# Kernel optimization log

Hardware: AMD Instinct MI355X
Metric: run time of the kernel (lower is better)

Reference implementation:

```python
import jax, jax.numpy as jnp
import numpy as np

GROUP_SIZE = 64

def _dequant_w4(qweight, wscales):
    """Unpack int4 weights and apply per-(group, out-channel) scales.
    qweight: [N, K//2] uint8-valued ints, low nibble = even k, high nibble = odd k.
    wscales: [K//GROUP_SIZE, N] float. Returns [N, K] float weight.
    """
    q = qweight.astype(jnp.int32)
    low = (q & 15) - 8          # [N, K//2], signed int4
    high = ((q >> 4) & 15) - 8  # [N, K//2]
    N = q.shape[0]
    K = q.shape[1] * 2
    w_int = jnp.stack([low, high], axis=-1).reshape(N, K)  # interleaved low/high
    # scale[n, k] = wscales[k // GROUP_SIZE, n]
    scale = jnp.repeat(wscales, GROUP_SIZE, axis=0).T  # [N, K]
    return w_int.astype(wscales.dtype) * scale

def setup_inputs() -> dict:
    key = jax.random.key(0)
    ks = jax.random.split(key, 7)
    M, K, N, R = 8192, 4096, 4096, 32
    x = jax.random.normal(ks[0], (M, K), dtype=jnp.float32)
    qweight = jax.random.randint(ks[1], (N, K // 2), 0, 256, dtype=jnp.int32)
    wscales = jax.random.uniform(ks[2], (K // GROUP_SIZE, N), dtype=jnp.float32) * 0.01 + 0.001
    proj_down = jax.random.normal(ks[3], (R, K), dtype=jnp.float32) * 0.02
    proj_up = jax.random.normal(ks[4], (N, R), dtype=jnp.float32) * 0.02
    wtscale = jnp.ones((1,), dtype=jnp.float32)
    bias = jax.random.normal(ks[5], (N,), dtype=jnp.float32) * 0.01
    return {"x": x, "qweight": qweight, "wscales": wscales,
            "proj_down": proj_down, "proj_up": proj_up,
            "wtscale": wtscale, "bias": bias}

def reference(x, qweight, wscales, proj_down, proj_up, wtscale, bias):
    # Dequant int4 weight, GEMM, low-rank LoRA correction scaled by wtscale, bias.
    w = _dequant_w4(qweight, wscales)              # [N, K]
    out = x @ w.T                                  # [M, N]
    lora = (x @ proj_down.T) @ proj_up.T           # [M, R] @ [R, N] -> [M, N]
    out = out + lora * wtscale
    out = out + bias
    return out
```

## Files before the change

kernel.cpp:

```cpp
#include <hip/hip_runtime.h>
#include <hip/hip_bf16.h>
#include <stdint.h>

#define MD 8192
#define ND 4096
#define KD 4096
#define RD 32

typedef __bf16 bf16x8 __attribute__((ext_vector_type(8)));
typedef float f32x4 __attribute__((ext_vector_type(4)));

__device__ __forceinline__ void cp16(const void* g, void* l) {
    __builtin_amdgcn_global_load_lds(
        (const __attribute__((address_space(1))) void*)g,
        (__attribute__((address_space(3))) void*)l, 16, 0, 0);
}

__global__ __launch_bounds__(256) void cvt_x(const float* __restrict__ x,
                                             __hip_bfloat16* __restrict__ y) {
    size_t i = ((size_t)blockIdx.x * 256 + threadIdx.x) * 8;
    float4 a = *(const float4*)(x + i);
    float4 b = *(const float4*)(x + i + 4);
    union { __hip_bfloat16 h[8]; uint4 u; } o;
    o.h[0] = __float2bfloat16(a.x); o.h[1] = __float2bfloat16(a.y);
    o.h[2] = __float2bfloat16(a.z); o.h[3] = __float2bfloat16(a.w);
    o.h[4] = __float2bfloat16(b.x); o.h[5] = __float2bfloat16(b.y);
    o.h[6] = __float2bfloat16(b.z); o.h[7] = __float2bfloat16(b.w);
    *(uint4*)(y + i) = o.u;
}

__global__ __launch_bounds__(256) void build_weff(
    const int* __restrict__ qw,
    const float* __restrict__ wsc,
    const float* __restrict__ pd,
    const float* __restrict__ pu,
    const float* __restrict__ wts_p,
    __hip_bfloat16* __restrict__ weff)
{
    __shared__ float pd_s[RD][132];
    __shared__ float pu_t[RD][68];
    const int t = threadIdx.x;
    const int kb = blockIdx.x * 128;
    const int nb = blockIdx.y * 64;

    for (int f = t; f < (RD * 128) / 4; f += 256) {
        int r = f >> 5;
        int c = (f & 31) << 2;
        *(float4*)&pd_s[r][c] = *(const float4*)(pd + (size_t)r * KD + kb + c);
    }
    for (int f = t; f < (64 * RD) / 4; f += 256) {
        int nl = f >> 3;
        int r4 = (f & 7) << 2;
        float4 v = *(const float4*)(pu + (size_t)(nb + nl) * RD + r4);
        pu_t[r4 + 0][nl] = v.x; pu_t[r4 + 1][nl] = v.y;
        pu_t[r4 + 2][nl] = v.z; pu_t[r4 + 3][nl] = v.w;
    }
    __syncthreads();

    const float wts = wts_p[0];
    const int kc = (t & 15) << 3;
    const int ng = (t >> 4) << 2;

    float acc[4][8];
#pragma unroll
    for (int i = 0; i < 4; ++i)
#pragma unroll
        for (int j = 0; j < 8; ++j) acc[i][j] = 0.f;

    for (int r = 0; r < RD; ++r) {
        float4 pda = *(const float4*)&pd_s[r][kc];
        float4 pdb = *(const float4*)&pd_s[r][kc + 4];
        float4 puv = *(const float4*)&pu_t[r][ng];
        float pus[4] = {puv.x, puv.y, puv.z, puv.w};
        float pdv[8] = {pda.x, pda.y, pda.z, pda.w, pdb.x, pdb.y, pdb.z, pdb.w};
#pragma unroll
        for (int i = 0; i < 4; ++i)
#pragma unroll
            for (int j = 0; j < 8; ++j)
                acc[i][j] += pus[i] * pdv[j];
    }

    const int kg = kb + kc;
    const int g = kg >> 6;
#pragma unroll
    for (int i = 0; i < 4; ++i) {
        const int n = nb + ng + i;
        const float sc = wsc[(size_t)g * ND + n];
        int4 q = *(const int4*)(qw + (size_t)n * (KD / 2) + (kg >> 1));
        const int qi[4] = {q.x, q.y, q.z, q.w};
        union { __hip_bfloat16 h[8]; uint4 u; } o;
#pragma unroll
        for (int j = 0; j < 4; ++j) {
            const int lo = (qi[j] & 15) - 8;
            const int hi = ((qi[j] >> 4) & 15) - 8;
            o.h[2 * j]     = __float2bfloat16((float)lo * sc + wts * acc[i][2 * j]);
            o.h[2 * j + 1] = __float2bfloat16((float)hi * sc + wts * acc[i][2 * j + 1]);
        }
        *(uint4*)(weff + (size_t)n * KD + kg) = o.u;
    }
}

#define FENCE asm volatile("" ::: "memory")

#define PHASEH(CB, SL)                                                         \
    {                                                                          \
        bf16x8 af[8], bf[4];                                                   \
        _Pragma("unroll") for (int i = 0; i < 8; ++i)                          \
            af[i] = *(const bf16x8*)(ArowB + (CB) + i * 2048 + (SL));          \
        _Pragma("unroll") for (int j = 0; j < 4; ++j)                          \
            bf[j] = *(const bf16x8*)(BrowB + (CB) + j * 2048 + (SL));          \
        asm volatile("s_waitcnt lgkmcnt(0)" ::: "memory");                     \
        __builtin_amdgcn_sched_barrier(0);                                     \
        __builtin_amdgcn_s_setprio(1);                                         \
        _Pragma("unroll") for (int i = 0; i < 8; ++i)                          \
            _Pragma("unroll") for (int j = 0; j < 4; ++j)                      \
                acc[i][j] = __builtin_amdgcn_mfma_f32_16x16x32_bf16(           \
                    af[i], bf[j], acc[i][j], 0, 0, 0);                         \
        __builtin_amdgcn_s_setprio(0);                                         \
    }

__global__ __launch_bounds__(512, 2) void gemm_bt_bias(
    const __hip_bfloat16* __restrict__ A,
    const __hip_bfloat16* __restrict__ B,
    const float* __restrict__ bias,
    float* __restrict__ C)
{
    __shared__ alignas(16) char As[2][32768];
    __shared__ alignas(16) char Bs[2][32768];

    const int t = threadIdx.x;
    const int lane = t & 63;
    const int w = t >> 6;
    const int wm = w >> 2;
    const int wn = w & 3;

    const int bid = blockIdx.x;
    const int swz = (bid & 7) * 64 + (bid >> 3);
    const int m0 = (swz >> 4) * 256;
    const int n0 = (swz & 15) * 256;

    const int lrow = lane >> 3;
    const int gch = (lane & 7) ^ lrow;
    const __hip_bfloat16* Ag = A + (size_t)(m0 + lrow) * KD + gch * 8;
    const __hip_bfloat16* Bg = B + (size_t)(n0 + lrow) * KD + gch * 8;

    const int qm = lane & 15;
    const int c4 = lane >> 4;
    const int slh0 = (c4 ^ (qm & 7)) * 16;
    const int slh1 = ((4 + c4) ^ (qm & 7)) * 16;
    const char* ArowB = (const char*)As + (wm * 128 + qm) * 128;
    const char* BrowB = (const char*)Bs + (wn * 64 + qm) * 128;

    f32x4 acc[8][4];
#pragma unroll
    for (int i = 0; i < 8; ++i)
#pragma unroll
        for (int j = 0; j < 4; ++j) acc[i][j] = (f32x4){0.f, 0.f, 0.f, 0.f};

#pragma unroll
    for (int q = 0; q < 4; ++q) {
        const int blk = w + 8 * q;
        cp16(Ag + (size_t)blk * 8 * KD, (char*)As + blk * 1024);
        cp16(Bg + (size_t)blk * 8 * KD, (char*)Bs + blk * 1024);
    }
    asm volatile("s_waitcnt vmcnt(0)" ::: "memory");
    __builtin_amdgcn_s_barrier();
    FENCE;

    for (int kt = 0; kt < 63; ++kt) {
        const int cb = (kt & 1) << 15;
        const int sb = cb ^ 32768;
        const size_t ko = (size_t)(kt + 1) * 64;
#pragma unroll
        for (int q = 0; q < 4; ++q) {
            const int blk = w + 8 * q;
            cp16(Ag + (size_t)blk * 8 * KD + ko, (char*)As + sb + blk * 1024);
            cp16(Bg + (size_t)blk * 8 * KD + ko, (char*)Bs + sb + blk * 1024);
        }
        PHASEH(cb, slh0)
        PHASEH(cb, slh1)
        asm volatile("s_waitcnt vmcnt(0)" ::: "memory");
        __builtin_amdgcn_s_barrier();
        FENCE;
    }
    PHASEH(32768, slh0)
    PHASEH(32768, slh1)

    const int cm = (lane >> 4) << 2;
    const int cn = lane & 15;
#pragma unroll
    for (int j = 0; j < 4; ++j) {
        const int n = n0 + wn * 64 + j * 16 + cn;
        const float bv = bias[n];
#pragma unroll
        for (int i = 0; i < 8; ++i) {
            float* dst = C + (size_t)(m0 + wm * 128 + i * 16 + cm) * ND + n;
#pragma unroll
            for (int r = 0; r < 4; ++r)
                dst[(size_t)r * ND] = acc[i][j][r] + bv;
        }
    }
}

extern "C" void kernel_launch(void* const* d_in, const int* in_sizes, int n_in,
                              void* d_out, int out_size, void* d_ws, size_t ws_size,
                              hipStream_t stream) {
    const float* x    = (const float*)d_in[0];
    const int* qw     = (const int*)d_in[1];
    const float* wsc  = (const float*)d_in[2];
    const float* pd   = (const float*)d_in[3];
    const float* pu   = (const float*)d_in[4];
    const float* wts  = (const float*)d_in[5];
    const float* bias = (const float*)d_in[6];
    float* out = (float*)d_out;

    __hip_bfloat16* weff = (__hip_bfloat16*)d_ws;
    __hip_bfloat16* xbf  = (__hip_bfloat16*)((char*)d_ws + (size_t)ND * KD * sizeof(__hip_bfloat16));

    cvt_x<<<(MD * (size_t)KD) / (256 * 8), 256, 0, stream>>>(x, xbf);
    build_weff<<<dim3(KD / 128, ND / 64), 256, 0, stream>>>(qw, wsc, pd, pu, wts, weff);
    gemm_bt_bias<<<512, 512, 0, stream>>>(xbf, weff, bias, out);
}
```

Before: 553.7 us.

## Split GEMM k-loop into quadrant phases interleaving loads, barriers and MFMAs

Restructures the main bf16 GEMM loop into four quadrant phases. Each phase issues a subset of the next tile's global-to-LDS copies, waits with partial vmcnt and a barrier, then runs a quarter of the MFMAs. This spreads memory traffic and synchronisation across the compute instead of a single wait at the end of each k-step. It adds more barriers per iteration, and the correctness of the per-quadrant wait counts and buffer reuse is delicate.

```diff
diff --git a/kernel.cpp b/kernel.cpp
--- a/kernel.cpp
+++ b/kernel.cpp
@@ -101,23 +101,34 @@
 }
 
 #define FENCE asm volatile("" ::: "memory")
-
-#define PHASEH(CB, SL)                                                         \
-    {                                                                          \
-        bf16x8 af[8], bf[4];                                                   \
-        _Pragma("unroll") for (int i = 0; i < 8; ++i)                          \
-            af[i] = *(const bf16x8*)(ArowB + (CB) + i * 2048 + (SL));          \
-        _Pragma("unroll") for (int j = 0; j < 4; ++j)                          \
-            bf[j] = *(const bf16x8*)(BrowB + (CB) + j * 2048 + (SL));          \
-        asm volatile("s_waitcnt lgkmcnt(0)" ::: "memory");                     \
-        __builtin_amdgcn_sched_barrier(0);                                     \
-        __builtin_amdgcn_s_setprio(1);                                         \
-        _Pragma("unroll") for (int i = 0; i < 8; ++i)                          \
-            _Pragma("unroll") for (int j = 0; j < 4; ++j)                      \
-                acc[i][j] = __builtin_amdgcn_mfma_f32_16x16x32_bf16(           \
-                    af[i], bf[j], acc[i][j], 0, 0, 0);                         \
-        __builtin_amdgcn_s_setprio(0);                                         \
-    }
+#define BAR __builtin_amdgcn_s_barrier()
+#define VMC(N) asm volatile("s_waitcnt vmcnt(" #N ")" ::: "memory")
+#define LGKM0                                                \
+    asm volatile("s_waitcnt lgkmcnt(0)" ::: "memory");       \
+    __builtin_amdgcn_sched_barrier(0)
+
+#define RD_AF(DST, G, CB)                                                      \
+    _Pragma("unroll") for (int i = 0; i < 4; ++i) {                            \
+        DST[i][0] = *(const bf16x8*)(ArowB + (CB) + ((G)*4 + i) * 2048 + slh0);\
+        DST[i][1] = *(const bf16x8*)(ArowB + (CB) + ((G)*4 + i) * 2048 + slh1);\
+    }
+#define RD_BF(DST, G, CB)                                                      \
+    _Pragma("unroll") for (int j = 0; j < 2; ++j) {                            \
+        DST[j][0] = *(const bf16x8*)(BrowB + (CB) + ((G)*2 + j) * 2048 + slh0);\
+        DST[j][1] = *(const bf16x8*)(BrowB + (CB) + ((G)*2 + j) * 2048 + slh1);\
+    }
+#define MFMAQ(MQ, NQ, AF, BF)                                                  \
+    __builtin_amdgcn_s_setprio(1);                                             \
+    _Pragma("unroll") for (int i = 0; i < 4; ++i)                              \
+        _Pragma("unroll") for (int j = 0; j < 2; ++j) {                        \
+            acc[(MQ)*4 + i][(NQ)*2 + j] =                                      \
+                __builtin_amdgcn_mfma_f32_16x16x32_bf16(                       \
+                    AF[i][0], BF[j][0], acc[(MQ)*4 + i][(NQ)*2 + j], 0, 0, 0); \
+            acc[(MQ)*4 + i][(NQ)*2 + j] =                                      \
+                __builtin_amdgcn_mfma_f32_16x16x32_bf16(                       \
+                    AF[i][1], BF[j][1], acc[(MQ)*4 + i][(NQ)*2 + j], 0, 0, 0); \
+        }                                                                      \
+    __builtin_amdgcn_s_setprio(0)
 
 __global__ __launch_bounds__(512, 2) void gemm_bt_bias(
     const __hip_bfloat16* __restrict__ A,
@@ -144,6 +155,12 @@
     const __hip_bfloat16* Ag = A + (size_t)(m0 + lrow) * KD + gch * 8;
     const __hip_bfloat16* Bg = B + (size_t)(n0 + lrow) * KD + gch * 8;
 
+    const int ap1a = w,      ap1b = 16 + w;
+    const int bp2a = (w & 3) + ((w >> 2) << 3);
+    const int bp2b = bp2a + 16;
+    const int ap3a = 8 + w,  ap3b = 24 + w;
+    const int bp4a = bp2a + 4, bp4b = bp2b + 4;
+
     const int qm = lane & 15;
     const int c4 = lane >> 4;
     const int slh0 = (c4 ^ (qm & 7)) * 16;
@@ -157,34 +174,70 @@
 #pragma unroll
         for (int j = 0; j < 4; ++j) acc[i][j] = (f32x4){0.f, 0.f, 0.f, 0.f};
 
-#pragma unroll
-    for (int q = 0; q < 4; ++q) {
-        const int blk = w + 8 * q;
-        cp16(Ag + (size_t)blk * 8 * KD, (char*)As + blk * 1024);
-        cp16(Bg + (size_t)blk * 8 * KD, (char*)Bs + blk * 1024);
-    }
-    asm volatile("s_waitcnt vmcnt(0)" ::: "memory");
-    __builtin_amdgcn_s_barrier();
+    cp16(Ag + (size_t)ap1a * 8 * KD, (char*)As + ap1a * 1024);
+    cp16(Ag + (size_t)ap1b * 8 * KD, (char*)As + ap1b * 1024);
+    cp16(Bg + (size_t)bp2a * 8 * KD, (char*)Bs + bp2a * 1024);
+    cp16(Bg + (size_t)bp2b * 8 * KD, (char*)Bs + bp2b * 1024);
+    cp16(Ag + (size_t)ap3a * 8 * KD, (char*)As + ap3a * 1024);
+    cp16(Ag + (size_t)ap3b * 8 * KD, (char*)As + ap3b * 1024);
+    cp16(Bg + (size_t)bp4a * 8 * KD, (char*)Bs + bp4a * 1024);
+    cp16(Bg + (size_t)bp4b * 8 * KD, (char*)Bs + bp4b * 1024);
+    VMC(4);
+    BAR;
     FENCE;
 
     for (int kt = 0; kt < 63; ++kt) {
         const int cb = (kt & 1) << 15;
         const int sb = cb ^ 32768;
         const size_t ko = (size_t)(kt + 1) * 64;
-#pragma unroll
-        for (int q = 0; q < 4; ++q) {
-            const int blk = w + 8 * q;
-            cp16(Ag + (size_t)blk * 8 * KD + ko, (char*)As + sb + blk * 1024);
-            cp16(Bg + (size_t)blk * 8 * KD + ko, (char*)Bs + sb + blk * 1024);
-        }
-        PHASEH(cb, slh0)
-        PHASEH(cb, slh1)
-        asm volatile("s_waitcnt vmcnt(0)" ::: "memory");
-        __builtin_amdgcn_s_barrier();
+        bf16x8 af0[4][2], af1[4][2], bf[2][2];
+        RD_AF(af0, 0, cb)
+        RD_BF(bf, 0, cb)
+        cp16(Ag + (size_t)ap1a * 8 * KD + ko, (char*)As + sb + ap1a * 1024);
+        cp16(Ag + (size_t)ap1b * 8 * KD + ko, (char*)As + sb + ap1b * 1024);
+        VMC(4);
+        BAR;
+        LGKM0;
+        MFMAQ(0, 0, af0, bf);
+        RD_AF(af1, 1, cb)
+        cp16(Bg + (size_t)bp2a * 8 * KD + ko, (char*)Bs + sb + bp2a * 1024);
+        cp16(Bg + (size_t)bp2b * 8 * KD + ko, (char*)Bs + sb + bp2b * 1024);
+        VMC(4);
+        BAR;
+        LGKM0;
+        MFMAQ(1, 0, af1, bf);
+        RD_BF(bf, 1, cb)
+        cp16(Ag + (size_t)ap3a * 8 * KD + ko, (char*)As + sb + ap3a * 1024);
+        cp16(Ag + (size_t)ap3b * 8 * KD + ko, (char*)As + sb + ap3b * 1024);
         FENCE;
-    }
-    PHASEH(32768, slh0)
-    PHASEH(32768, slh1)
+        BAR;
+        LGKM0;
+        MFMAQ(1, 1, af1, bf);
+        cp16(Bg + (size_t)bp4a * 8 * KD + ko, (char*)Bs + sb + bp4a * 1024);
+        cp16(Bg + (size_t)bp4b * 8 * KD + ko, (char*)Bs + sb + bp4b * 1024);
+        VMC(4);
+        BAR;
+        MFMAQ(0, 1, af0, bf);
+    }
+    {
+        const int cb = 32768;
+        bf16x8 af0[4][2], af1[4][2], bf[2][2];
+        RD_AF(af0, 0, cb)
+        RD_BF(bf, 0, cb)
+        VMC(2);
+        BAR;
+        LGKM0;
+        MFMAQ(0, 0, af0, bf);
+        RD_AF(af1, 1, cb)
+        VMC(0);
+        BAR;
+        LGKM0;
+        MFMAQ(1, 0, af1, bf);
+        RD_BF(bf, 1, cb)
+        LGKM0;
+        MFMAQ(1, 1, af1, bf);
+        MFMAQ(0, 1, af0, bf);
+    }
 
     const int cm = (lane >> 4) << 2;
     const int cn = lane & 15;
```

Result: faster. 515.7 us (-6.9%).
